# Kernel optimization log

Hardware: AMD Instinct MI355X
Metric: run time of the kernel (lower is better)

Reference implementation:

```python
import jax, jax.numpy as jnp
import numpy as np

B, S, HID, NH, HD, NL = 2, 4096, 1024, 16, 64, 128
N_ITER = 6


def setup_inputs() -> dict:
    key = jax.random.key(0)
    ks = jax.random.split(key, 9)
    s = 0.02
    D = NH * HD
    return {
        "X": jax.random.normal(ks[0], (B, S, HID), jnp.float32),
        "mask": jnp.ones((B, S), jnp.float32),
        "Wq": jax.random.normal(ks[1], (HID, D), jnp.float32) * s,
        "bq": jnp.zeros((D,), jnp.float32),
        "Wk": jax.random.normal(ks[2], (HID, D), jnp.float32) * s,
        "bk": jnp.zeros((D,), jnp.float32),
        "Wv": jax.random.normal(ks[3], (HID, D), jnp.float32) * s,
        "bv": jnp.zeros((D,), jnp.float32),
        "Wo": jax.random.normal(ks[4], (D, HID), jnp.float32) * s,
        "bo": jnp.zeros((HID,), jnp.float32),
    }


def iterative_inv(mat, n_iter=N_ITER):
    # Newton-Schulz style pseudo-inverse iteration (Nystromformer 'original' init)
    I = jnp.eye(mat.shape[-1], dtype=mat.dtype)
    K = mat
    V = K.swapaxes(-1, -2) / jnp.max(jnp.sum(K, axis=-2))
    for _ in range(n_iter):
        KV = K @ V
        V = 0.25 * V @ (13.0 * I - KV @ (15.0 * I - KV @ (7.0 * I - KV)))
    return V


def nystrom_core(Q, K, V, mask):
    # Q,K,V: [B,NH,S,HD], mask: [B,S]
    scale = 1.0 / np.sqrt(np.sqrt(HD))  # 1/d^(1/4) applied to both Q and K
    m = mask[:, None, :, None]
    Q = Q * m * scale
    K = K * m * scale
    seg = S // NL
    # landmarks: mean over contiguous segments -> [B,NH,NL,HD]
    Ql = Q.reshape(B, NH, NL, seg, HD).mean(axis=-2)
    Kl = K.reshape(B, NH, NL, seg, HD).mean(axis=-2)
    k1 = jax.nn.softmax(jnp.einsum('bhsd,bhld->bhsl', Q, Kl), axis=-1)   # [B,NH,S,NL]
    k2 = jax.nn.softmax(jnp.einsum('bhld,bhmd->bhlm', Ql, Kl), axis=-1)  # [B,NH,NL,NL]
    k3 = jax.nn.softmax(
        jnp.einsum('bhld,bhsd->bhls', Ql, K) - 1e9 * (1.0 - mask[:, None, None, :]),
        axis=-1)                                                          # [B,NH,NL,S]
    return k1 @ iterative_inv(k2) @ (k3 @ V)                              # [B,NH,S,HD]


def reference(X, mask, Wq, bq, Wk, bk, Wv, bv, Wo, bo):
    def split(Y):  # [B,S,NH*HD] -> [B,NH,S,HD]
        return Y.reshape(B, S, NH, HD).transpose(0, 2, 1, 3)
    Q = split(X @ Wq + bq)
    K = split(X @ Wk + bk)
    V = split(X @ Wv + bv)
    attn = nystrom_core(Q.astype(jnp.float32), K.astype(jnp.float32),
                        V.astype(jnp.float32), mask.astype(jnp.float32))
    out = attn.transpose(0, 2, 1, 3).reshape(B, S, NH * HD)
    return out @ Wo + bo
```

## Files before the change

### kernel.cpp

```cpp
#include <hip/hip_runtime.h>
#include <math.h>

constexpr int cB = 2, cS = 4096, cHID = 1024, cNH = 16, cHD = 64, cNL = 128, cSEG = 32, cD = 1024, cBH = 32;
constexpr float cSCALE = 0.35355339059327373f;

typedef _Float16 f16x8 __attribute__((ext_vector_type(8)));
typedef float f32x4 __attribute__((ext_vector_type(4)));

__device__ inline void gload_lds16(const void* g, void* l) {
    __builtin_amdgcn_global_load_lds(
        (const __attribute__((address_space(1))) void*)g,
        (__attribute__((address_space(3))) void*)l, 16, 0, 0);
}

__global__ __launch_bounds__(256) void cast_x(const float* __restrict__ X, _Float16* __restrict__ Xh)
{
    int i = (blockIdx.x * 256 + threadIdx.x) * 4;
    float4 v = *reinterpret_cast<const float4*>(X + i);
    union { _Float16 h[4]; ushort4 u; } p;
    p.h[0] = (_Float16)v.x; p.h[1] = (_Float16)v.y; p.h[2] = (_Float16)v.z; p.h[3] = (_Float16)v.w;
    *reinterpret_cast<ushort4*>(Xh + i) = p.u;
}

__global__ __launch_bounds__(256) void wcast_t(
    const float* __restrict__ Wq, const float* __restrict__ Wk,
    const float* __restrict__ Wv, const float* __restrict__ Wo,
    _Float16* __restrict__ WqT, _Float16* __restrict__ WkT,
    _Float16* __restrict__ WvT, _Float16* __restrict__ WoT)
{
    __shared__ float tile[32][33];
    const int wsel = blockIdx.z;
    const float* W = (wsel == 0) ? Wq : (wsel == 1 ? Wk : (wsel == 2 ? Wv : Wo));
    _Float16* WT   = (wsel == 0) ? WqT : (wsel == 1 ? WkT : (wsel == 2 ? WvT : WoT));
    const int n0 = blockIdx.x * 32, k0 = blockIdx.y * 32;
    const int t = threadIdx.x;
    const int r = t >> 3, c = (t & 7) * 4;
    float4 v = *reinterpret_cast<const float4*>(W + (size_t)(k0 + r) * cD + n0 + c);
    tile[r][c] = v.x; tile[r][c + 1] = v.y; tile[r][c + 2] = v.z; tile[r][c + 3] = v.w;
    __syncthreads();
    union { _Float16 h[4]; ushort4 u; } p;
    p.h[0] = (_Float16)tile[c + 0][r]; p.h[1] = (_Float16)tile[c + 1][r];
    p.h[2] = (_Float16)tile[c + 2][r]; p.h[3] = (_Float16)tile[c + 3][r];
    *reinterpret_cast<ushort4*>(WT + (size_t)(n0 + r) * cHID + k0 + c) = p.u;
}

__global__ __launch_bounds__(256) void xm_kernel(
    const float* __restrict__ X, const float* __restrict__ mask,
    float* __restrict__ Xm, float* __restrict__ mbar)
{
    const int bl = blockIdx.x;
    const int b = bl >> 7, l = bl & 127;
    const int c = threadIdx.x * 4;
    float4 a = {0.f, 0.f, 0.f, 0.f};
    float msum = 0.f;
    for (int j = 0; j < cSEG; ++j) {
        float m = mask[b * cS + l * cSEG + j];
        float4 x = *reinterpret_cast<const float4*>(X + ((size_t)(b * cS + l * cSEG + j)) * cHID + c);
        a.x += m * x.x; a.y += m * x.y; a.z += m * x.z; a.w += m * x.w;
        msum += m;
    }
    const float inv = 1.0f / cSEG;
    a.x *= inv; a.y *= inv; a.z *= inv; a.w *= inv;
    *reinterpret_cast<float4*>(Xm + (size_t)bl * cHID + c) = a;
    if (threadIdx.x == 0) mbar[bl] = msum * inv;
}

__global__ __launch_bounds__(256) void qkv_gemm_f16(
    const _Float16* __restrict__ Xh, const float* __restrict__ mask,
    const _Float16* __restrict__ WqT, const _Float16* __restrict__ WkT, const _Float16* __restrict__ WvT,
    const float* __restrict__ bq, const float* __restrict__ bk, const float* __restrict__ bv,
    _Float16* __restrict__ Qh, _Float16* __restrict__ Kh, _Float16* __restrict__ Vh)
{
    __shared__ __align__(16) _Float16 As[128 * 64];
    __shared__ __align__(16) _Float16 Bs[128 * 64];
    const int wsel = blockIdx.z;
    const _Float16* WT = (wsel == 0) ? WqT : (wsel == 1 ? WkT : WvT);
    const float* bias  = (wsel == 0) ? bq  : (wsel == 1 ? bk  : bv);
    _Float16* Y        = (wsel == 0) ? Qh  : (wsel == 1 ? Kh  : Vh);
    const int orig = blockIdx.x;
    const int xcd = orig & 7, idx = orig >> 3;
    const int n0 = (idx & 7) * 128;
    const int m0 = (xcd * 8 + (idx >> 3)) * 128;
    const int t = threadIdx.x;
    const int wave = t >> 6, lane = t & 63;
    const int wm = (wave >> 1) * 64, wn = (wave & 1) * 64;
    const int quad = lane >> 4, l15 = lane & 15;
    const int srow = wave * 8 + (lane >> 3);
    const int scol = ((lane & 7) ^ (lane >> 3)) * 8;

    f32x4 acc[4][4];
#pragma unroll
    for (int i = 0; i < 4; ++i)
#pragma unroll
        for (int j = 0; j < 4; ++j) acc[i][j] = (f32x4){0.f, 0.f, 0.f, 0.f};

    for (int k0 = 0; k0 < cHID; k0 += 64) {
        const _Float16* aSrc = Xh + (size_t)(m0 + srow) * cHID + k0 + scol;
        const _Float16* bSrc = WT + (size_t)(n0 + srow) * cHID + k0 + scol;
#pragma unroll
        for (int i = 0; i < 4; ++i) {
            gload_lds16(aSrc + (size_t)(i * 32) * cHID, &As[(wave * 8 + i * 32) * 64]);
            gload_lds16(bSrc + (size_t)(i * 32) * cHID, &Bs[(wave * 8 + i * 32) * 64]);
        }
        __syncthreads();
        f16x8 af[2][4], bf[2][4];
#pragma unroll
        for (int kh = 0; kh < 2; ++kh) {
            const int cg = ((kh * 4 + quad) ^ (l15 & 7)) * 8;
#pragma unroll
            for (int mt = 0; mt < 4; ++mt)
                af[kh][mt] = *reinterpret_cast<const f16x8*>(&As[(wm + mt * 16 + l15) * 64 + cg]);
#pragma unroll
            for (int nt = 0; nt < 4; ++nt)
                bf[kh][nt] = *reinterpret_cast<const f16x8*>(&Bs[(wn + nt * 16 + l15) * 64 + cg]);
        }
#pragma unroll
        for (int kh = 0; kh < 2; ++kh)
#pragma unroll
            for (int mt = 0; mt < 4; ++mt)
#pragma unroll
                for (int nt = 0; nt < 4; ++nt)
                    acc[mt][nt] = __builtin_amdgcn_mfma_f32_16x16x32_f16(af[kh][mt], bf[kh][nt], acc[mt][nt], 0, 0, 0);
        __syncthreads();
    }
#pragma unroll
    for (int mt = 0; mt < 4; ++mt) {
#pragma unroll
        for (int r = 0; r < 4; ++r) {
            int R = m0 + wm + mt * 16 + quad * 4 + r;
            int b = R >> 12, s = R & (cS - 1);
            float msc = (wsel < 2) ? mask[b * cS + s] * cSCALE : 1.0f;
#pragma unroll
            for (int nt = 0; nt < 4; ++nt) {
                int Cc = n0 + wn + nt * 16 + l15;
                int h = Cc >> 6, d = Cc & 63;
                float val = (acc[mt][nt][r] + bias[Cc]) * msc;
                Y[((size_t)(b * cNH + h) * cS + s) * cHD + d] = (_Float16)val;
            }
        }
    }
}

__global__ __launch_bounds__(256) void out_gemm_f16(
    const _Float16* __restrict__ Ah, const _Float16* __restrict__ WT,
    const float* __restrict__ bias, float* __restrict__ Y)
{
    __shared__ __align__(16) _Float16 As[128 * 64];
    __shared__ __align__(16) _Float16 Bs[128 * 64];
    const int orig = blockIdx.x;
    const int xcd = orig & 7, idx = orig >> 3;
    const int n0 = (idx & 7) * 128;
    const int m0 = (xcd * 8 + (idx >> 3)) * 128;
    const int t = threadIdx.x;
    const int wave = t >> 6, lane = t & 63;
    const int wm = (wave >> 1) * 64, wn = (wave & 1) * 64;
    const int quad = lane >> 4, l15 = lane & 15;
    const int srow = wave * 8 + (lane >> 3);
    const int scol = ((lane & 7) ^ (lane >> 3)) * 8;

    f32x4 acc[4][4];
#pragma unroll
    for (int i = 0; i < 4; ++i)
#pragma unroll
        for (int j = 0; j < 4; ++j) acc[i][j] = (f32x4){0.f, 0.f, 0.f, 0.f};

    for (int k0 = 0; k0 < cD; k0 += 64) {
        const _Float16* aSrc = Ah + (size_t)(m0 + srow) * cD + k0 + scol;
        const _Float16* bSrc = WT + (size_t)(n0 + srow) * cD + k0 + scol;
#pragma unroll
        for (int i = 0; i < 4; ++i) {
            gload_lds16(aSrc + (size_t)(i * 32) * cD, &As[(wave * 8 + i * 32) * 64]);
            gload_lds16(bSrc + (size_t)(i * 32) * cD, &Bs[(wave * 8 + i * 32) * 64]);
        }
        __syncthreads();
        f16x8 af[2][4], bf[2][4];
#pragma unroll
        for (int kh = 0; kh < 2; ++kh) {
            const int cg = ((kh * 4 + quad) ^ (l15 & 7)) * 8;
#pragma unroll
            for (int mt = 0; mt < 4; ++mt)
                af[kh][mt] = *reinterpret_cast<const f16x8*>(&As[(wm + mt * 16 + l15) * 64 + cg]);
#pragma unroll
            for (int nt = 0; nt < 4; ++nt)
                bf[kh][nt] = *reinterpret_cast<const f16x8*>(&Bs[(wn + nt * 16 + l15) * 64 + cg]);
        }
#pragma unroll
        for (int kh = 0; kh < 2; ++kh)
#pragma unroll
            for (int mt = 0; mt < 4; ++mt)
#pragma unroll
                for (int nt = 0; nt < 4; ++nt)
                    acc[mt][nt] = __builtin_amdgcn_mfma_f32_16x16x32_f16(af[kh][mt], bf[kh][nt], acc[mt][nt], 0, 0, 0);
        __syncthreads();
    }
#pragma unroll
    for (int mt = 0; mt < 4; ++mt) {
#pragma unroll
        for (int r = 0; r < 4; ++r) {
            int R = m0 + wm + mt * 16 + quad * 4 + r;
#pragma unroll
            for (int nt = 0; nt < 4; ++nt) {
                int Cc = n0 + wn + nt * 16 + l15;
                Y[(size_t)R * cHID + Cc] = acc[mt][nt][r] + bias[Cc];
            }
        }
    }
}

__global__ __launch_bounds__(256) void lgemm(
    const float* __restrict__ Xm, const float* __restrict__ mbar,
    const float* __restrict__ Wq, const float* __restrict__ bq,
    const float* __restrict__ Wk, const float* __restrict__ bk,
    float* __restrict__ Ql, float* __restrict__ Kl,
    _Float16* __restrict__ Qlh, _Float16* __restrict__ Klh)
{
    __shared__ __align__(16) float As[16][68];
    __shared__ __align__(16) float Bs[16][68];
    const int tid = threadIdx.x;
    const int wsel = blockIdx.z;
    const float* W    = wsel ? Wk : Wq;
    const float* bias = wsel ? bk : bq;
    float* Yl         = wsel ? Kl : Ql;
    _Float16* Ylh     = wsel ? Klh : Qlh;
    const int c0 = blockIdx.x * 64, r0 = blockIdx.y * 64;
    const int tx = tid & 15, ty = tid >> 4;
    const int am = tid >> 2, ak = (tid & 3) * 4;
    const int bkk = tid >> 4, bn = (tid & 15) * 4;

    float acc[4][4] = {};
    for (int k0 = 0; k0 < cHID; k0 += 16) {
        float4 a4 = *reinterpret_cast<const float4*>(Xm + (size_t)(r0 + am) * cHID + k0 + ak);
        As[ak + 0][am] = a4.x; As[ak + 1][am] = a4.y; As[ak + 2][am] = a4.z; As[ak + 3][am] = a4.w;
        float4 b4 = *reinterpret_cast<const float4*>(W + (size_t)(k0 + bkk) * cD + c0 + bn);
        *reinterpret_cast<float4*>(&Bs[bkk][bn]) = b4;
        __syncthreads();
#pragma unroll
        for (int kk = 0; kk < 16; ++kk) {
            float4 av  = *reinterpret_cast<const float4*>(&As[kk][ty * 4]);
            float4 bv4 = *reinterpret_cast<const float4*>(&Bs[kk][tx * 4]);
            float a_[4] = {av.x, av.y, av.z, av.w};
            float b_[4] = {bv4.x, bv4.y, bv4.z, bv4.w};
#pragma unroll
            for (int i = 0; i < 4; ++i)
#pragma unroll
                for (int j = 0; j < 4; ++j) acc[i][j] += a_[i] * b_[j];
        }
        __syncthreads();
    }
#pragma unroll
    for (int i = 0; i < 4; ++i) {
        int r = r0 + ty * 4 + i;
        int b = r >> 7, l = r & 127;
        float mb = mbar[r];
#pragma unroll
        for (int j = 0; j < 4; ++j) {
            int c = c0 + tx * 4 + j;
            int h = c >> 6, d = c & 63;
            float val = (acc[i][j] + mb * bias[c]) * cSCALE;
            size_t idx = ((size_t)(b * cNH + h) * cNL + l) * cHD + d;
            Yl[idx] = val;
            Ylh[idx] = (_Float16)val;
        }
    }
}

__global__ __launch_bounds__(128) void k2_softmax(
    const float* __restrict__ Ql, const float* __restrict__ Kl, float* __restrict__ k2)
{
    __shared__ __align__(16) float qrow[64];
    __shared__ float red[128];
    int bh = blockIdx.x >> 7, i = blockIdx.x & 127;
    int j = threadIdx.x;
    if (j < 64) qrow[j] = Ql[(bh * cNL + i) * cHD + j];
    __syncthreads();
    const float4* q4  = reinterpret_cast<const float4*>(qrow);
    const float4* kl4 = reinterpret_cast<const float4*>(Kl + (bh * cNL + j) * cHD);
    float dot = 0.f;
#pragma unroll
    for (int u = 0; u < 16; ++u) {
        float4 a = q4[u], b = kl4[u];
        dot += a.x * b.x + a.y * b.y + a.z * b.z + a.w * b.w;
    }
    red[j] = dot; __syncthreads();
    for (int off = 64; off > 0; off >>= 1) { if (j < off) red[j] = fmaxf(red[j], red[j + off]); __syncthreads(); }
    float m = red[0]; __syncthreads();
    float e = expf(dot - m);
    red[j] = e; __syncthreads();
    for (int off = 64; off > 0; off >>= 1) { if (j < off) red[j] += red[j + off]; __syncthreads(); }
    k2[(bh * cNL + i) * cNL + j] = e / red[0];
}

__global__ __launch_bounds__(128) void colsum_max(const float* __restrict__ k2, int* __restrict__ cmax)
{
    __shared__ float red[128];
    int bh = blockIdx.x, j = threadIdx.x;
    float s = 0.f;
    for (int i = 0; i < cNL; ++i) s += k2[(bh * cNL + i) * cNL + j];
    red[j] = s; __syncthreads();
    for (int off = 64; off > 0; off >>= 1) { if (j < off) red[j] = fmaxf(red[j], red[j + off]); __syncthreads(); }
    if (j == 0) atomicMax(cmax, __float_as_int(red[0]));
}

__device__ inline void split2(float v, _Float16& h, _Float16& l) {
    h = (_Float16)v;
    l = (_Float16)(v - (float)h);
}
__device__ inline unsigned short f16bits(_Float16 h) { return __builtin_bit_cast(unsigned short, h); }

#define NYS_MFMA(a, b, c) __builtin_amdgcn_mfma_f32_16x16x32_f16((a), (b), (c), 0, 0, 0)

#define NYS_PRELOAD(PH, PL, LH, LL)                                                     \
    {                                                                                   \
        _Pragma("unroll")                                                               \
        for (int mt_ = 0; mt_ < 2; ++mt_) {                                             \
            const int rowL_ = wr * 32 + mt_ * 16 + l15;                                 \
            _Pragma("unroll")                                                           \
            for (int k0_ = 0; k0_ < 4; ++k0_) {                                         \
                LH[mt_][k0_] = *reinterpret_cast<const f16x8*>(&PH[rowL_ * 136 + k0_ * 32 + quad * 8]); \
                LL[mt_][k0_] = *reinterpret_cast<const f16x8*>(&PL[rowL_ * 136 + k0_ * 32 + quad * 8]); \
            }                                                                           \
        }                                                                               \
    }

#define NYS_PRODUCT(PH, PL, LH, LL)                                                     \
    {                                                                                   \
        _Pragma("unroll")                                                               \
        for (int nt_ = 0; nt_ < 4; ++nt_) {                                             \
            f32x4 a0_ = (f32x4){0.f, 0.f, 0.f, 0.f};                                    \
            f32x4 a1_ = (f32x4){0.f, 0.f, 0.f, 0.f};                                    \
            _Pragma("unroll")                                                           \
            for (int k0_ = 0; k0_ < 4; ++k0_) {                                         \
                const int boff_ = (wcb + nt_ * 16) * 136 + k0_ * 32 + quad * 8;         \
                f16x8 bh_ = *reinterpret_cast<const f16x8*>(&PH[boff_]);                \
                f16x8 bl_ = *reinterpret_cast<const f16x8*>(&PL[boff_]);                \
                a0_ = NYS_MFMA(LH[0][k0_], bh_, a0_);                                   \
                a1_ = NYS_MFMA(LH[1][k0_], bh_, a1_);                                   \
                a0_ = NYS_MFMA(LL[0][k0_], bh_, a0_);                                   \
                a1_ = NYS_MFMA(LL[1][k0_], bh_, a1_);                                   \
                a0_ = NYS_MFMA(LH[0][k0_], bl_, a0_);                                   \
                a1_ = NYS_MFMA(LH[1][k0_], bl_, a1_);                                   \
            }                                                                           \
            acc[0][nt_] = a0_; acc[1][nt_] = a1_;                                       \
        }                                                                               \
    }

__global__ __launch_bounds__(512, 2) void nys_fused(
    const float* __restrict__ k2, const int* __restrict__ cmax,
    float* __restrict__ Mg0, float* __restrict__ Mg1)
{
    __shared__ __align__(16) _Float16 Ahi_s[128 * 136];
    __shared__ __align__(16) _Float16 Alo_s[128 * 136];
    __shared__ __align__(16) _Float16 Whi_s[128 * 136];
    __shared__ __align__(16) _Float16 Wlo_s[128 * 136];
    const int bh = blockIdx.x;
    const int t = threadIdx.x;
    const int wave = t >> 6, lane = t & 63;
    const int wr = wave >> 1, wc = wave & 1;
    const int quad = lane >> 4, l15 = lane & 15;
    const int wcb = wc * 64 + l15;
    const float* Kg = k2 + (size_t)bh * 16384;
    float* Mg0b = Mg0 + (size_t)bh * 16384;
    float* Mg1b = Mg1 + (size_t)bh * 16384;
    const float sc = sqrtf(1.0f / __int_as_float(*cmax));

    {
        const int row = t >> 2, c0 = (t & 3) * 32;
        const float* src = Kg + row * 128 + c0;
        _Float16* dh = &Whi_s[row * 136 + c0];
        _Float16* dl = &Wlo_s[row * 136 + c0];
#pragma unroll
        for (int u = 0; u < 32; u += 4) {
            float4 v = *reinterpret_cast<const float4*>(src + u);
            ushort4 ph, pl; _Float16 h, l;
            split2(v.x * sc, h, l); ph.x = f16bits(h); pl.x = f16bits(l);
            split2(v.y * sc, h, l); ph.y = f16bits(h); pl.y = f16bits(l);
            split2(v.z * sc, h, l); ph.z = f16bits(h); pl.z = f16bits(l);
            split2(v.w * sc, h, l); ph.w = f16bits(h); pl.w = f16bits(l);
            *reinterpret_cast<ushort4*>(dh + u) = ph;
            *reinterpret_cast<ushort4*>(dl + u) = pl;
        }
    }
    __syncthreads();

    f32x4 acc[2][4];
    f16x8 Fh[2][4], Fl[2][4];

    NYS_PRELOAD(Whi_s, Wlo_s, Fh, Fl);
    NYS_PRODUCT(Whi_s, Wlo_s, Fh, Fl);
#pragma unroll
    for (int mt = 0; mt < 2; ++mt)
#pragma unroll
        for (int nt = 0; nt < 4; ++nt) {
            const int col = wcb + nt * 16;
            const int rb  = wr * 32 + mt * 16 + quad * 4;
            ushort4 ph, pl;
#pragma unroll
            for (int r = 0; r < 4; ++r) {
                _Float16 h, l; split2(acc[mt][nt][r], h, l);
                ((unsigned short*)&ph)[r] = f16bits(h);
                ((unsigned short*)&pl)[r] = f16bits(l);
            }
            *reinterpret_cast<ushort4*>(&Ahi_s[col * 136 + rb]) = ph;
            *reinterpret_cast<ushort4*>(&Alo_s[col * 136 + rb]) = pl;
        }
    __syncthreads();

    for (int it = 0; it < 6; ++it) {
        NYS_PRELOAD(Ahi_s, Alo_s, Fh, Fl);
        NYS_PRODUCT(Ahi_s, Alo_s, Fh, Fl);
#pragma unroll
        for (int mt = 0; mt < 2; ++mt)
#pragma unroll
            for (int nt = 0; nt < 4; ++nt) {
                const int col = wcb + nt * 16;
                const int rb  = wr * 32 + mt * 16 + quad * 4;
                ushort4 ah = *reinterpret_cast<const ushort4*>(&Ahi_s[col * 136 + rb]);
                ushort4 al = *reinterpret_cast<const ushort4*>(&Alo_s[col * 136 + rb]);
                ushort4 ph, pl;
#pragma unroll
                for (int r = 0; r < 4; ++r) {
                    float av = (float)__builtin_bit_cast(_Float16, ((unsigned short*)&ah)[r])
                             + (float)__builtin_bit_cast(_Float16, ((unsigned short*)&al)[r]);
                    float v = ((rb + r) == col ? 15.0f : 0.0f) - 7.0f * av + acc[mt][nt][r];
                    _Float16 h, l; split2(v, h, l);
                    ((unsigned short*)&ph)[r] = f16bits(h);
                    ((unsigned short*)&pl)[r] = f16bits(l);
                }
                *reinterpret_cast<ushort4*>(&Whi_s[col * 136 + rb]) = ph;
                *reinterpret_cast<ushort4*>(&Wlo_s[col * 136 + rb]) = pl;
            }
        __syncthreads();
        NYS_PRODUCT(Whi_s, Wlo_s, Fh, Fl);
        __syncthreads();
#pragma unroll
        for (int mt = 0; mt < 2; ++mt)
#pragma unroll
            for (int nt = 0; nt < 4; ++nt) {
                const int col = wcb + nt * 16;
                const int rb  = wr * 32 + mt * 16 + quad * 4;
                ushort4 ph, pl; float4 mv;
#pragma unroll
                for (int r = 0; r < 4; ++r) {
                    float v = ((rb + r) == col ? 13.0f : 0.0f) - acc[mt][nt][r];
                    _Float16 h, l; split2(v, h, l);
                    ((unsigned short*)&ph)[r] = f16bits(h);
                    ((unsigned short*)&pl)[r] = f16bits(l);
                    ((float*)&mv)[r] = 0.25f * v;
                }
                *reinterpret_cast<ushort4*>(&Whi_s[col * 136 + rb]) = ph;
                *reinterpret_cast<ushort4*>(&Wlo_s[col * 136 + rb]) = pl;
                if (it == 0)
                    *reinterpret_cast<float4*>(&Mg0b[col * 128 + rb]) = mv;
            }
        __syncthreads();
        NYS_PRODUCT(Whi_s, Wlo_s, Fh, Fl);
#pragma unroll
        for (int mt = 0; mt < 2; ++mt)
#pragma unroll
            for (int nt = 0; nt < 4; ++nt) {
                const int col = wcb + nt * 16;
                const int rb  = wr * 32 + mt * 16 + quad * 4;
                ushort4 ph, pl;
#pragma unroll
                for (int r = 0; r < 4; ++r) {
                    _Float16 h, l; split2(0.25f * acc[mt][nt][r], h, l);
                    ((unsigned short*)&ph)[r] = f16bits(h);
                    ((unsigned short*)&pl)[r] = f16bits(l);
                }
                *reinterpret_cast<ushort4*>(&Ahi_s[col * 136 + rb]) = ph;
                *reinterpret_cast<ushort4*>(&Alo_s[col * 136 + rb]) = pl;
            }
        if (it >= 1) {
            const float* Mr = (it & 1) ? Mg0b : Mg1b;
            float*       Mw = (it & 1) ? Mg1b : Mg0b;
            f16x8 Mh[2][4], Ml[2][4];
#pragma unroll
            for (int mt = 0; mt < 2; ++mt) {
                const int rowL = wr * 32 + mt * 16 + l15;
#pragma unroll
                for (int k0 = 0; k0 < 4; ++k0) {
                    const float* src = Mr + rowL * 128 + k0 * 32 + quad * 8;
                    float4 v0 = *reinterpret_cast<const float4*>(src);
                    float4 v1 = *reinterpret_cast<const float4*>(src + 4);
                    union { f16x8 v; _Float16 e[8]; } hh, ll;
                    split2(v0.x, hh.e[0], ll.e[0]); split2(v0.y, hh.e[1], ll.e[1]);
                    split2(v0.z, hh.e[2], ll.e[2]); split2(v0.w, hh.e[3], ll.e[3]);
                    split2(v1.x, hh.e[4], ll.e[4]); split2(v1.y, hh.e[5], ll.e[5]);
                    split2(v1.z, hh.e[6], ll.e[6]); split2(v1.w, hh.e[7], ll.e[7]);
                    Mh[mt][k0] = hh.v; Ml[mt][k0] = ll.v;
                }
            }
            NYS_PRODUCT(Whi_s, Wlo_s, Mh, Ml);
#pragma unroll
            for (int mt = 0; mt < 2; ++mt)
#pragma unroll
                for (int nt = 0; nt < 4; ++nt) {
                    const int col = wcb + nt * 16;
                    const int rb  = wr * 32 + mt * 16 + quad * 4;
                    float4 mv;
#pragma unroll
                    for (int r = 0; r < 4; ++r) ((float*)&mv)[r] = 0.25f * acc[mt][nt][r];
                    *reinterpret_cast<float4*>(&Mw[col * 128 + rb]) = mv;
                }
        }
        __syncthreads();
    }
}

__global__ __launch_bounds__(256) void vtrans(const _Float16* __restrict__ Vh, _Float16* __restrict__ VTh)
{
    __shared__ ushort T[64][72];
    const int s0 = blockIdx.x * 64, bh = blockIdx.y;
    const int t = threadIdx.x;
    const _Float16* vb = Vh + ((size_t)bh * cS + s0) * cHD;
#pragma unroll
    for (int i = 0; i < 2; ++i) {
        int idx = t + i * 256;
        int row = idx >> 3, c8 = idx & 7;
        f16x8 v = *reinterpret_cast<const f16x8*>(vb + (size_t)row * cHD + c8 * 8);
#pragma unroll
        for (int j = 0; j < 8; ++j) T[row][c8 * 8 + j] = ((ushort*)&v)[j];
    }
    __syncthreads();
    _Float16* vt = VTh + (size_t)bh * cHD * cS;
#pragma unroll
    for (int i = 0; i < 2; ++i) {
        int idx = t + i * 256;
        int d = idx >> 3, s8 = idx & 7;
        f16x8 o;
#pragma unroll
        for (int j = 0; j < 8; ++j) ((ushort*)&o)[j] = T[s8 * 8 + j][d];
        *reinterpret_cast<f16x8*>(vt + (size_t)d * cS + s0 + s8 * 8) = o;
    }
}

__global__ __launch_bounds__(256) void k3v_mfma(
    const _Float16* __restrict__ Qlh, const _Float16* __restrict__ Kh,
    const _Float16* __restrict__ VTh, const float* __restrict__ mask,
    float* __restrict__ Opart, float* __restrict__ mpart, float* __restrict__ spart)
{
    __shared__ __align__(16) _Float16 Ps[128 * 72];
    __shared__ float msk[256];
    const int z = blockIdx.x, bh = blockIdx.y;
    const int b = bh >> 4;
    const int sbase = z * 256;
    const int t = threadIdx.x;
    const int wave = t >> 6, lane = t & 63;
    const int quad = lane >> 4, l15 = lane & 15;

    msk[t] = mask[b * cS + sbase + t];

    f16x8 aq[2][2];
    const _Float16* qlg = Qlh + (size_t)bh * cNL * cHD;
#pragma unroll
    for (int mt = 0; mt < 2; ++mt)
#pragma unroll
        for (int k0 = 0; k0 < 2; ++k0)
            aq[mt][k0] = *reinterpret_cast<const f16x8*>(
                qlg + (size_t)(wave * 32 + mt * 16 + l15) * cHD + k0 * 32 + quad * 8);

    float mrun[2][4], srun[2][4];
    f32x4 accO[2][4];
#pragma unroll
    for (int mt = 0; mt < 2; ++mt)
#pragma unroll
        for (int r = 0; r < 4; ++r) { mrun[mt][r] = -1e30f; srun[mt][r] = 0.f; }
#pragma unroll
    for (int mt = 0; mt < 2; ++mt)
#pragma unroll
        for (int dt = 0; dt < 4; ++dt) accO[mt][dt] = (f32x4){0.f, 0.f, 0.f, 0.f};

    __syncthreads();

    const _Float16* kg = Kh + (size_t)bh * cS * cHD;
    const _Float16* vg = VTh + (size_t)bh * cHD * cS;

    for (int step = 0; step < 4; ++step) {
        const int st = sbase + step * 64;
        f32x4 accS[2][4];
#pragma unroll
        for (int mt = 0; mt < 2; ++mt)
#pragma unroll
            for (int nt = 0; nt < 4; ++nt) accS[mt][nt] = (f32x4){0.f, 0.f, 0.f, 0.f};
#pragma unroll
        for (int k0 = 0; k0 < 2; ++k0)
#pragma unroll
            for (int nt = 0; nt < 4; ++nt) {
                f16x8 bk = *reinterpret_cast<const f16x8*>(
                    kg + (size_t)(st + nt * 16 + l15) * cHD + k0 * 32 + quad * 8);
#pragma unroll
                for (int mt = 0; mt < 2; ++mt)
                    accS[mt][nt] = __builtin_amdgcn_mfma_f32_16x16x32_f16(aq[mt][k0], bk, accS[mt][nt], 0, 0, 0);
            }
#pragma unroll
        for (int nt = 0; nt < 4; ++nt) {
            float pen = 1e9f * (1.0f - msk[step * 64 + nt * 16 + l15]);
#pragma unroll
            for (int mt = 0; mt < 2; ++mt)
#pragma unroll
                for (int r = 0; r < 4; ++r) accS[mt][nt][r] -= pen;
        }
#pragma unroll
        for (int mt = 0; mt < 2; ++mt) {
#pragma unroll
            for (int r = 0; r < 4; ++r) {
                float tmax = fmaxf(fmaxf(accS[mt][0][r], accS[mt][1][r]),
                                   fmaxf(accS[mt][2][r], accS[mt][3][r]));
#pragma unroll
                for (int w = 1; w < 16; w <<= 1) tmax = fmaxf(tmax, __shfl_xor(tmax, w, 16));
                float mnew = fmaxf(mrun[mt][r], tmax);
                float alpha = __expf(mrun[mt][r] - mnew);
                float ts = 0.f;
#pragma unroll
                for (int nt = 0; nt < 4; ++nt) {
                    float e = __expf(accS[mt][nt][r] - mnew);
                    accS[mt][nt][r] = e; ts += e;
                }
#pragma unroll
                for (int w = 1; w < 16; w <<= 1) ts += __shfl_xor(ts, w, 16);
                srun[mt][r] = srun[mt][r] * alpha + ts;
                mrun[mt][r] = mnew;
#pragma unroll
                for (int dt = 0; dt < 4; ++dt) accO[mt][dt][r] *= alpha;
            }
        }
#pragma unroll
        for (int mt = 0; mt < 2; ++mt)
#pragma unroll
            for (int nt = 0; nt < 4; ++nt)
#pragma unroll
                for (int r = 0; r < 4; ++r)
                    Ps[(wave * 32 + mt * 16 + quad * 4 + r) * 72 + nt * 16 + l15] =
                        (_Float16)accS[mt][nt][r];
#pragma unroll
        for (int k0 = 0; k0 < 2; ++k0) {
            f16x8 ap[2];
#pragma unroll
            for (int mt = 0; mt < 2; ++mt)
                ap[mt] = *reinterpret_cast<const f16x8*>(
                    &Ps[(wave * 32 + mt * 16 + l15) * 72 + k0 * 32 + quad * 8]);
#pragma unroll
            for (int dt = 0; dt < 4; ++dt) {
                f16x8 bv = *reinterpret_cast<const f16x8*>(
                    vg + (size_t)(dt * 16 + l15) * cS + st + k0 * 32 + quad * 8);
#pragma unroll
                for (int mt = 0; mt < 2; ++mt)
                    accO[mt][dt] = __builtin_amdgcn_mfma_f32_16x16x32_f16(ap[mt], bv, accO[mt][dt], 0, 0, 0);
            }
        }
    }
    const int rowbase = bh * cNL + wave * 32;
#pragma unroll
    for (int mt = 0; mt < 2; ++mt)
#pragma unroll
        for (int dt = 0; dt < 4; ++dt)
#pragma unroll
            for (int r = 0; r < 4; ++r)
                Opart[(size_t)(z * 4096 + rowbase + mt * 16 + quad * 4 + r) * cHD + dt * 16 + l15] =
                    accO[mt][dt][r];
    if (l15 == 0) {
#pragma unroll
        for (int mt = 0; mt < 2; ++mt)
#pragma unroll
            for (int r = 0; r < 4; ++r) {
                int prow = z * 4096 + rowbase + mt * 16 + quad * 4 + r;
                mpart[prow] = mrun[mt][r];
                spart[prow] = srun[mt][r];
            }
    }
}

__global__ __launch_bounds__(256) void k3v_reduce(
    const float* __restrict__ Opart, const float* __restrict__ mpart,
    const float* __restrict__ spart, float* __restrict__ CV)
{
    const int t = threadIdx.x;
    const int row = blockIdx.x * 4 + (t >> 6);
    const int d = t & 63;
    float mstar = -1e30f;
#pragma unroll
    for (int z = 0; z < 16; ++z) mstar = fmaxf(mstar, mpart[z * 4096 + row]);
    float ssum = 0.f, acc = 0.f;
#pragma unroll
    for (int z = 0; z < 16; ++z) {
        float w = __expf(mpart[z * 4096 + row] - mstar);
        ssum += w * spart[z * 4096 + row];
        acc  += w * Opart[(size_t)(z * 4096 + row) * cHD + d];
    }
    CV[(size_t)row * cHD + d] = acc / ssum;
}

__global__ __launch_bounds__(256) void w2_matmul(
    const float* __restrict__ k2, const float* __restrict__ M6,
    const int* __restrict__ cmax, const float* __restrict__ CV,
    _Float16* __restrict__ W2T)
{
    __shared__ __align__(16) float CVs[128][68];
    __shared__ __align__(16) float Us[128][68];
    const int bh = blockIdx.x, t = threadIdx.x;
    const float invc = 1.0f / __int_as_float(*cmax);
    for (int k = 0; k < 32; ++k) { int idx = t + k * 256; CVs[idx >> 6][idx & 63] = CV[(size_t)bh * 8192 + idx]; }
    __syncthreads();
    const float* Mg = M6 + (size_t)bh * 16384;
    {
        const int tx = t & 15, ty = t >> 4;
        float acc[8][4] = {};
        for (int k = 0; k < 128; ++k) {
            float4 b4 = *reinterpret_cast<const float4*>(&CVs[k][tx * 4]);
#pragma unroll
            for (int i = 0; i < 8; ++i) {
                float a = Mg[(ty * 8 + i) * 128 + k];
                acc[i][0] += a * b4.x; acc[i][1] += a * b4.y; acc[i][2] += a * b4.z; acc[i][3] += a * b4.w;
            }
        }
#pragma unroll
        for (int i = 0; i < 8; ++i)
#pragma unroll
            for (int j = 0; j < 4; ++j)
                Us[ty * 8 + i][tx * 4 + j] = acc[i][j];
    }
    __syncthreads();
    {
        const int l = t & 127, dg = (t >> 7) * 32;
        float acc2[32];
#pragma unroll
        for (int dd = 0; dd < 32; ++dd) acc2[dd] = 0.f;
        const float* kg = k2 + (size_t)bh * 16384;
        for (int j = 0; j < 128; ++j) {
            float kv = kg[j * 128 + l];
#pragma unroll
            for (int dd = 0; dd < 32; ++dd) acc2[dd] += kv * Us[j][dg + dd];
        }
        _Float16* wt = W2T + (size_t)bh * (cHD * cNL);
#pragma unroll
        for (int dd = 0; dd < 32; ++dd)
            wt[(size_t)(dg + dd) * cNL + l] = (_Float16)(acc2[dd] * invc);
    }
}

__global__ __launch_bounds__(256) void k1_mfma(
    const _Float16* __restrict__ Qh, const _Float16* __restrict__ Klh,
    const _Float16* __restrict__ W2T, _Float16* __restrict__ ctxh)
{
    __shared__ __align__(16) _Float16 Qs[64 * 72];
    __shared__ __align__(16) _Float16 Ps[64 * 136];
    const int s0 = blockIdx.x * 64, bh = blockIdx.y;
    const int b = bh >> 4, h = bh & 15;
    const int t = threadIdx.x;
    const int wave = t >> 6, lane = t & 63;
    const int quad = lane >> 4, l15 = lane & 15;

    {
        const _Float16* qg = Qh + ((size_t)bh * cS + s0) * cHD;
#pragma unroll
        for (int i = 0; i < 2; ++i) {
            int idx = t + i * 256;
            int row = idx >> 3, c8 = idx & 7;
            *reinterpret_cast<f16x8*>(&Qs[row * 72 + c8 * 8]) =
                *reinterpret_cast<const f16x8*>(qg + (size_t)row * cHD + c8 * 8);
        }
    }
    __syncthreads();

    const _Float16* klg = Klh + (size_t)bh * cNL * cHD;
    f32x4 accS[8];
#pragma unroll
    for (int nt = 0; nt < 8; ++nt) accS[nt] = (f32x4){0.f, 0.f, 0.f, 0.f};
#pragma unroll
    for (int k0 = 0; k0 < 2; ++k0) {
        f16x8 aq = *reinterpret_cast<const f16x8*>(&Qs[(wave * 16 + l15) * 72 + k0 * 32 + quad * 8]);
#pragma unroll
        for (int nt = 0; nt < 8; ++nt) {
            f16x8 bk = *reinterpret_cast<const f16x8*>(klg + (size_t)(nt * 16 + l15) * cHD + k0 * 32 + quad * 8);
            accS[nt] = __builtin_amdgcn_mfma_f32_16x16x32_f16(aq, bk, accS[nt], 0, 0, 0);
        }
    }

    float rmax[4] = {-1e30f, -1e30f, -1e30f, -1e30f};
#pragma unroll
    for (int nt = 0; nt < 8; ++nt)
#pragma unroll
        for (int r = 0; r < 4; ++r) rmax[r] = fmaxf(rmax[r], accS[nt][r]);
#pragma unroll
    for (int r = 0; r < 4; ++r)
#pragma unroll
        for (int w = 1; w < 16; w <<= 1) rmax[r] = fmaxf(rmax[r], __shfl_xor(rmax[r], w, 16));
    float rsum[4] = {0.f, 0.f, 0.f, 0.f};
#pragma unroll
    for (int nt = 0; nt < 8; ++nt)
#pragma unroll
        for (int r = 0; r < 4; ++r) { accS[nt][r] = __expf(accS[nt][r] - rmax[r]); rsum[r] += accS[nt][r]; }
#pragma unroll
    for (int r = 0; r < 4; ++r) {
#pragma unroll
        for (int w = 1; w < 16; w <<= 1) rsum[r] += __shfl_xor(rsum[r], w, 16);
        rsum[r] = 1.0f / rsum[r];
    }
#pragma unroll
    for (int nt = 0; nt < 8; ++nt)
#pragma unroll
        for (int r = 0; r < 4; ++r)
            Ps[(wave * 16 + quad * 4 + r) * 136 + nt * 16 + l15] = (_Float16)(accS[nt][r] * rsum[r]);
    __syncthreads();

    const _Float16* wtg = W2T + (size_t)bh * cHD * cNL;
    f32x4 accO[4];
#pragma unroll
    for (int nt = 0; nt < 4; ++nt) accO[nt] = (f32x4){0.f, 0.f, 0.f, 0.f};
#pragma unroll
    for (int k0 = 0; k0 < 4; ++k0) {
        f16x8 ap = *reinterpret_cast<const f16x8*>(&Ps[(wave * 16 + l15) * 136 + k0 * 32 + quad * 8]);
#pragma unroll
        for (int nt = 0; nt < 4; ++nt) {
            f16x8 bw = *reinterpret_cast<const f16x8*>(wtg + (size_t)(nt * 16 + l15) * cNL + k0 * 32 + quad * 8);
            accO[nt] = __builtin_amdgcn_mfma_f32_16x16x32_f16(ap, bw, accO[nt], 0, 0, 0);
        }
    }
#pragma unroll
    for (int nt = 0; nt < 4; ++nt)
#pragma unroll
        for (int r = 0; r < 4; ++r) {
            int s = s0 + wave * 16 + quad * 4 + r;
            int d = nt * 16 + l15;
            ctxh[((size_t)(b * cS) + s) * cD + h * cHD + d] = (_Float16)accO[nt][r];
        }
}

extern "C" void kernel_launch(void* const* d_in, const int* in_sizes, int n_in,
                              void* d_out, int out_size, void* d_ws, size_t ws_size,
                              hipStream_t stream)
{
    const float* X    = (const float*)d_in[0];
    const float* mask = (const float*)d_in[1];
    const float* Wq   = (const float*)d_in[2];
    const float* bq   = (const float*)d_in[3];
    const float* Wk   = (const float*)d_in[4];
    const float* bk   = (const float*)d_in[5];
    const float* Wv   = (const float*)d_in[6];
    const float* bv   = (const float*)d_in[7];
    const float* Wo   = (const float*)d_in[8];
    const float* bo   = (const float*)d_in[9];
    float* out = (float*)d_out;

    float* ws = (float*)d_ws;
    size_t off = 0;
    const size_t szQKV = (size_t)cBH * cS * cHD;
    const size_t szL   = (size_t)cBH * cNL * cHD;
    const size_t szM   = (size_t)cBH * cNL * cNL;
    float* Qr   = ws + off; off += szQKV;
    float* Kr   = ws + off; off += szQKV;
    float* Vr   = ws + off; off += szQKV;
    _Float16* Xh  = (_Float16*)(ws + off); off += szQKV / 2;
    _Float16* WqT = (_Float16*)(ws + off); off += 524288;
    _Float16* WkT = (_Float16*)(ws + off); off += 524288;
    _Float16* WvT = (_Float16*)(ws + off); off += 524288;
    _Float16* WoT = (_Float16*)(ws + off); off += 524288;
    float* Xm   = ws + off; off += (size_t)cB * cNL * cHID;
    float* mbar = ws + off; off += 256;
    float* Ql  = ws + off; off += szL;
    float* Kl  = ws + off; off += szL;
    float* k2  = ws + off; off += szM;
    float* Mg0 = ws + off; off += szM;
    float* Mg1 = ws + off; off += szM;
    float* Zb  = ws + off; off += szM;
    float* T2b = ws + off; off += szM;
    float* T3b = ws + off; off += szM;
    float* CV  = ws + off; off += szL;
    _Float16* Qlh  = (_Float16*)(ws + off); off += szL / 2;
    _Float16* Klh  = (_Float16*)(ws + off); off += szL / 2;
    _Float16* W2Th = (_Float16*)(ws + off); off += szL / 2;
    int*   cmax = (int*)(ws + off); off += 16;
    float* mpart = ws + off; off += 65536;
    float* spart = ws + off; off += 65536;

    _Float16* Qh   = (_Float16*)Qr;
    float*    Opart = Qr + szQKV / 2;
    _Float16* Kh   = (_Float16*)Kr;
    _Float16* ctxh = (_Float16*)(Kr + szQKV / 2);
    _Float16* Vh   = (_Float16*)Vr;
    _Float16* VTh  = (_Float16*)(Vr + szQKV / 2);

    (void)Zb; (void)T2b; (void)T3b;

    hipMemsetAsync(cmax, 0, sizeof(int), stream);

    cast_x<<<(int)(szQKV / 1024), 256, 0, stream>>>(X, Xh);
    wcast_t<<<dim3(32, 32, 4), 256, 0, stream>>>(Wq, Wk, Wv, Wo, WqT, WkT, WvT, WoT);
    xm_kernel<<<cB * cNL, 256, 0, stream>>>(X, mask, Xm, mbar);

    qkv_gemm_f16<<<dim3(512, 1, 3), 256, 0, stream>>>(
        Xh, mask, WqT, WkT, WvT, bq, bk, bv, Qh, Kh, Vh);
    vtrans<<<dim3(cS / 64, cBH), 256, 0, stream>>>(Vh, VTh);
    lgemm<<<dim3(cD / 64, (cB * cNL) / 64, 2), 256, 0, stream>>>(Xm, mbar, Wq, bq, Wk, bk, Ql, Kl, Qlh, Klh);

    k2_softmax<<<cBH * cNL, 128, 0, stream>>>(Ql, Kl, k2);
    colsum_max<<<cBH, 128, 0, stream>>>(k2, cmax);

    nys_fused<<<cBH, 512, 0, stream>>>(k2, cmax, Mg0, Mg1);

    k3v_mfma<<<dim3(16, cBH), 256, 0, stream>>>(Qlh, Kh, VTh, mask, Opart, mpart, spart);
    k3v_reduce<<<1024, 256, 0, stream>>>(Opart, mpart, spart, CV);
    w2_matmul<<<cBH, 256, 0, stream>>>(k2, Mg1, cmax, CV, W2Th);
    k1_mfma<<<dim3(cS / 64, cBH), 256, 0, stream>>>(Qh, Klh, W2Th, ctxh);
    out_gemm_f16<<<dim3(512), 256, 0, stream>>>(ctxh, WoT, bo, out);
}
```

Baseline: 473.2 us.

## Fuse X fp16 cast into landmark-mean kernel and retile Nystrom inverse waves

The separate cast_x kernel is removed, and xm_kernel now writes the fp16 copy of X while it already reads X for the segment means. This saves one full pass over X and one launch. Separately, the nys_fused Newton-Schulz kernel changes its wave layout from 4x2 to 2x4. Each wave now computes a 64x32 tile instead of 32x64, which changes how A-fragments and B-loads are reused from LDS and raises register use for the preloaded fragments.

New measurement: 474.2 us. Within noise of the previous version (+0.2%).

```diff
diff --git a/kernel.cpp b/kernel.cpp
--- a/kernel.cpp
+++ b/kernel.cpp
@@ -11,15 +11,6 @@
     __builtin_amdgcn_global_load_lds(
         (const __attribute__((address_space(1))) void*)g,
         (__attribute__((address_space(3))) void*)l, 16, 0, 0);
-}
-
-__global__ __launch_bounds__(256) void cast_x(const float* __restrict__ X, _Float16* __restrict__ Xh)
-{
-    int i = (blockIdx.x * 256 + threadIdx.x) * 4;
-    float4 v = *reinterpret_cast<const float4*>(X + i);
-    union { _Float16 h[4]; ushort4 u; } p;
-    p.h[0] = (_Float16)v.x; p.h[1] = (_Float16)v.y; p.h[2] = (_Float16)v.z; p.h[3] = (_Float16)v.w;
-    *reinterpret_cast<ushort4*>(Xh + i) = p.u;
 }
 
 __global__ __launch_bounds__(256) void wcast_t(
@@ -46,7 +37,7 @@
 
 __global__ __launch_bounds__(256) void xm_kernel(
     const float* __restrict__ X, const float* __restrict__ mask,
-    float* __restrict__ Xm, float* __restrict__ mbar)
+    float* __restrict__ Xm, float* __restrict__ mbar, _Float16* __restrict__ Xh)
 {
     const int bl = blockIdx.x;
     const int b = bl >> 7, l = bl & 127;
@@ -55,7 +46,12 @@
     float msum = 0.f;
     for (int j = 0; j < cSEG; ++j) {
         float m = mask[b * cS + l * cSEG + j];
-        float4 x = *reinterpret_cast<const float4*>(X + ((size_t)(b * cS + l * cSEG + j)) * cHID + c);
+        size_t roff = ((size_t)(b * cS + l * cSEG + j)) * cHID + c;
+        float4 x = *reinterpret_cast<const float4*>(X + roff);
+        union { _Float16 h[4]; ushort4 u; } p;
+        p.h[0] = (_Float16)x.x; p.h[1] = (_Float16)x.y;
+        p.h[2] = (_Float16)x.z; p.h[3] = (_Float16)x.w;
+        *reinterpret_cast<ushort4*>(Xh + roff) = p.u;
         a.x += m * x.x; a.y += m * x.y; a.z += m * x.z; a.w += m * x.w;
         msum += m;
     }
@@ -312,8 +308,8 @@
 #define NYS_PRELOAD(PH, PL, LH, LL)                                                     \
     {                                                                                   \
         _Pragma("unroll")                                                               \
-        for (int mt_ = 0; mt_ < 2; ++mt_) {                                             \
-            const int rowL_ = wr * 32 + mt_ * 16 + l15;                                 \
+        for (int mt_ = 0; mt_ < 4; ++mt_) {                                             \
+            const int rowL_ = wr * 64 + mt_ * 16 + l15;                                 \
             _Pragma("unroll")                                                           \
             for (int k0_ = 0; k0_ < 4; ++k0_) {                                         \
                 LH[mt_][k0_] = *reinterpret_cast<const f16x8*>(&PH[rowL_ * 136 + k0_ * 32 + quad * 8]); \
@@ -325,22 +321,23 @@
 #define NYS_PRODUCT(PH, PL, LH, LL)                                                     \
     {                                                                                   \
         _Pragma("unroll")                                                               \
-        for (int nt_ = 0; nt_ < 4; ++nt_) {                                             \
-            f32x4 a0_ = (f32x4){0.f, 0.f, 0.f, 0.f};                                    \
-            f32x4 a1_ = (f32x4){0.f, 0.f, 0.f, 0.f};                                    \
+        for (int mt_ = 0; mt_ < 4; ++mt_)                                               \
+            _Pragma("unroll")                                                           \
+            for (int nt_ = 0; nt_ < 2; ++nt_) acc[mt_][nt_] = (f32x4){0.f, 0.f, 0.f, 0.f}; \
+        _Pragma("unroll")                                                               \
+        for (int nt_ = 0; nt_ < 2; ++nt_) {                                             \
             _Pragma("unroll")                                                           \
             for (int k0_ = 0; k0_ < 4; ++k0_) {                                         \
                 const int boff_ = (wcb + nt_ * 16) * 136 + k0_ * 32 + quad * 8;         \
                 f16x8 bh_ = *reinterpret_cast<const f16x8*>(&PH[boff_]);                \
                 f16x8 bl_ = *reinterpret_cast<const f16x8*>(&PL[boff_]);                \
-                a0_ = NYS_MFMA(LH[0][k0_], bh_, a0_);                                   \
-                a1_ = NYS_MFMA(LH[1][k0_], bh_, a1_);                                   \
-                a0_ = NYS_MFMA(LL[0][k0_], bh_, a0_);                                   \
-                a1_ = NYS_MFMA(LL[1][k0_], bh_, a1_);                                   \
-                a0_ = NYS_MFMA(LH[0][k0_], bl_, a0_);                                   \
-                a1_ = NYS_MFMA(LH[1][k0_], bl_, a1_);                                   \
+                _Pragma("unroll")                                                       \
+                for (int mt_ = 0; mt_ < 4; ++mt_) {                                     \
+                    acc[mt_][nt_] = NYS_MFMA(LH[mt_][k0_], bh_, acc[mt_][nt_]);         \
+                    acc[mt_][nt_] = NYS_MFMA(LL[mt_][k0_], bh_, acc[mt_][nt_]);         \
+                    acc[mt_][nt_] = NYS_MFMA(LH[mt_][k0_], bl_, acc[mt_][nt_]);         \
+                }                                                                       \
             }                                                                           \
-            acc[0][nt_] = a0_; acc[1][nt_] = a1_;                                       \
         }                                                                               \
     }
 
@@ -355,9 +352,9 @@
     const int bh = blockIdx.x;
     const int t = threadIdx.x;
     const int wave = t >> 6, lane = t & 63;
-    const int wr = wave >> 1, wc = wave & 1;
+    const int wr = wave >> 2, wc = wave & 3;
     const int quad = lane >> 4, l15 = lane & 15;
-    const int wcb = wc * 64 + l15;
+    const int wcb = wc * 32 + l15;
     const float* Kg = k2 + (size_t)bh * 16384;
     float* Mg0b = Mg0 + (size_t)bh * 16384;
     float* Mg1b = Mg1 + (size_t)bh * 16384;
@@ -382,17 +379,17 @@
     }
     __syncthreads();
 
-    f32x4 acc[2][4];
-    f16x8 Fh[2][4], Fl[2][4];
+    f32x4 acc[4][2];
+    f16x8 Fh[4][4], Fl[4][4];
 
     NYS_PRELOAD(Whi_s, Wlo_s, Fh, Fl);
     NYS_PRODUCT(Whi_s, Wlo_s, Fh, Fl);
 #pragma unroll
-    for (int mt = 0; mt < 2; ++mt)
-#pragma unroll
-        for (int nt = 0; nt < 4; ++nt) {
+    for (int mt = 0; mt < 4; ++mt)
+#pragma unroll
+        for (int nt = 0; nt < 2; ++nt) {
             const int col = wcb + nt * 16;
-            const int rb  = wr * 32 + mt * 16 + quad * 4;
+            const int rb  = wr * 64 + mt * 16 + quad * 4;
             ushort4 ph, pl;
 #pragma unroll
             for (int r = 0; r < 4; ++r) {
@@ -409,11 +406,11 @@
         NYS_PRELOAD(Ahi_s, Alo_s, Fh, Fl);
         NYS_PRODUCT(Ahi_s, Alo_s, Fh, Fl);
 #pragma unroll
-        for (int mt = 0; mt < 2; ++mt)
-#pragma unroll
-            for (int nt = 0; nt < 4; ++nt) {
+        for (int mt = 0; mt < 4; ++mt)
+#pragma unroll
+            for (int nt = 0; nt < 2; ++nt) {
                 const int col = wcb + nt * 16;
-                const int rb  = wr * 32 + mt * 16 + quad * 4;
+                const int rb  = wr * 64 + mt * 16 + quad * 4;
                 ushort4 ah = *reinterpret_cast<const ushort4*>(&Ahi_s[col * 136 + rb]);
                 ushort4 al = *reinterpret_cast<const ushort4*>(&Alo_s[col * 136 + rb]);
                 ushort4 ph, pl;
@@ -433,11 +430,11 @@
         NYS_PRODUCT(Whi_s, Wlo_s, Fh, Fl);
         __syncthreads();
 #pragma unroll
-        for (int mt = 0; mt < 2; ++mt)
-#pragma unroll
-            for (int nt = 0; nt < 4; ++nt) {
+        for (int mt = 0; mt < 4; ++mt)
+#pragma unroll
+            for (int nt = 0; nt < 2; ++nt) {
                 const int col = wcb + nt * 16;
-                const int rb  = wr * 32 + mt * 16 + quad * 4;
+                const int rb  = wr * 64 + mt * 16 + quad * 4;
                 ushort4 ph, pl; float4 mv;
 #pragma unroll
                 for (int r = 0; r < 4; ++r) {
@@ -455,11 +452,11 @@
         __syncthreads();
         NYS_PRODUCT(Whi_s, Wlo_s, Fh, Fl);
 #pragma unroll
-        for (int mt = 0; mt < 2; ++mt)
-#pragma unroll
-            for (int nt = 0; nt < 4; ++nt) {
+        for (int mt = 0; mt < 4; ++mt)
+#pragma unroll
+            for (int nt = 0; nt < 2; ++nt) {
                 const int col = wcb + nt * 16;
-                const int rb  = wr * 32 + mt * 16 + quad * 4;
+                const int rb  = wr * 64 + mt * 16 + quad * 4;
                 ushort4 ph, pl;
 #pragma unroll
                 for (int r = 0; r < 4; ++r) {
@@ -473,12 +470,16 @@
         if (it >= 1) {
             const float* Mr = (it & 1) ? Mg0b : Mg1b;
             float*       Mw = (it & 1) ? Mg1b : Mg0b;
-            f16x8 Mh[2][4], Ml[2][4];
-#pragma unroll
-            for (int mt = 0; mt < 2; ++mt) {
-                const int rowL = wr * 32 + mt * 16 + l15;
-#pragma unroll
-                for (int k0 = 0; k0 < 4; ++k0) {
+#pragma unroll
+            for (int mt = 0; mt < 4; ++mt)
+#pragma unroll
+                for (int nt = 0; nt < 2; ++nt) acc[mt][nt] = (f32x4){0.f, 0.f, 0.f, 0.f};
+#pragma unroll
+            for (int k0 = 0; k0 < 4; ++k0) {
+                f16x8 Mh[4], Ml[4];
+#pragma unroll
+                for (int mt = 0; mt < 4; ++mt) {
+                    const int rowL = wr * 64 + mt * 16 + l15;
                     const float* src = Mr + rowL * 128 + k0 * 32 + quad * 8;
                     float4 v0 = *reinterpret_cast<const float4*>(src);
                     float4 v1 = *reinterpret_cast<const float4*>(src + 4);
@@ -487,16 +488,27 @@
                     split2(v0.z, hh.e[2], ll.e[2]); split2(v0.w, hh.e[3], ll.e[3]);
                     split2(v1.x, hh.e[4], ll.e[4]); split2(v1.y, hh.e[5], ll.e[5]);
                     split2(v1.z, hh.e[6], ll.e[6]); split2(v1.w, hh.e[7], ll.e[7]);
-                    Mh[mt][k0] = hh.v; Ml[mt][k0] = ll.v;
+                    Mh[mt] = hh.v; Ml[mt] = ll.v;
                 }
-            }
-            NYS_PRODUCT(Whi_s, Wlo_s, Mh, Ml);
-#pragma unroll
-            for (int mt = 0; mt < 2; ++mt)
-#pragma unroll
-                for (int nt = 0; nt < 4; ++nt) {
+#pragma unroll
+                for (int nt = 0; nt < 2; ++nt) {
+                    const int boff = (wcb + nt * 16) * 136 + k0 * 32 + quad * 8;
+                    f16x8 bh_ = *reinterpret_cast<const f16x8*>(&Whi_s[boff]);
+                    f16x8 bl_ = *reinterpret_cast<const f16x8*>(&Wlo_s[boff]);
+#pragma unroll
+                    for (int mt = 0; mt < 4; ++mt) {
+                        acc[mt][nt] = NYS_MFMA(Mh[mt], bh_, acc[mt][nt]);
+                        acc[mt][nt] = NYS_MFMA(Ml[mt], bh_, acc[mt][nt]);
+                        acc[mt][nt] = NYS_MFMA(Mh[mt], bl_, acc[mt][nt]);
+                    }
+                }
+            }
+#pragma unroll
+            for (int mt = 0; mt < 4; ++mt)
+#pragma unroll
+                for (int nt = 0; nt < 2; ++nt) {
                     const int col = wcb + nt * 16;
-                    const int rb  = wr * 32 + mt * 16 + quad * 4;
+                    const int rb  = wr * 64 + mt * 16 + quad * 4;
                     float4 mv;
 #pragma unroll
                     for (int r = 0; r < 4; ++r) ((float*)&mv)[r] = 0.25f * acc[mt][nt][r];
@@ -884,9 +896,8 @@
 
     hipMemsetAsync(cmax, 0, sizeof(int), stream);
 
-    cast_x<<<(int)(szQKV / 1024), 256, 0, stream>>>(X, Xh);
     wcast_t<<<dim3(32, 32, 4), 256, 0, stream>>>(Wq, Wk, Wv, Wo, WqT, WkT, WvT, WoT);
-    xm_kernel<<<cB * cNL, 256, 0, stream>>>(X, mask, Xm, mbar);
+    xm_kernel<<<cB * cNL, 256, 0, stream>>>(X, mask, Xm, mbar, Xh);
 
     qkv_gemm_f16<<<dim3(512, 1, 3), 256, 0, stream>>>(
         Xh, mask, WqT, WkT, WvT, bq, bk, bv, Qh, Kh, Vh);
```
